# Optimization experiments

Hardware: AMD Instinct MI355X
Metric: run time of the kernel (lower is better)

Reference implementation:

```python
import jax, jax.numpy as jnp
import numpy as np

KH = KW = 3
K = KH * KW
STRIDE = 1
PAD = 1
DIL = 1
GROUPS = 1
DG = 1  # deformable_groups
CIN = 256
COUT = 256
DC = 64  # depth_channels


def conv2d(x, w, b):
    out = jax.lax.conv_general_dilated(
        x, w, (STRIDE, STRIDE), [(PAD, PAD), (PAD, PAD)],
        rhs_dilation=(DIL, DIL), dimension_numbers=('NCHW', 'OIHW', 'NCHW'))
    return out + b[None, :, None, None]


def deform_sample(x, offset, mask):
    """Modulated deformable im2col. x:[N,C,H,W], offset:[N,DG*2*K,Ho,Wo],
    mask:[N,DG*K,Ho,Wo] or None. Returns cols [N,C,K,Ho,Wo]."""
    N, C, H, W = x.shape
    Ho = (H + 2 * PAD - (DIL * (KH - 1) + 1)) // STRIDE + 1
    Wo = (W + 2 * PAD - (DIL * (KW - 1) + 1)) // STRIDE + 1
    ky, kx = jnp.meshgrid(jnp.arange(KH), jnp.arange(KW), indexing='ij')
    # base sampling grid per kernel tap: [K,Ho,Wo]
    base_y = (jnp.arange(Ho) * STRIDE - PAD)[None, :, None] + (ky.reshape(-1) * DIL)[:, None, None]
    base_x = (jnp.arange(Wo) * STRIDE - PAD)[None, None, :] + (kx.reshape(-1) * DIL)[:, None, None]
    off = offset.reshape(N, DG, K, 2, Ho, Wo)  # [...,0]=dy, [...,1]=dx (CUDA layout)
    y = base_y[None, None].astype(x.dtype) + off[:, :, :, 0]
    xx = base_x[None, None].astype(x.dtype) + off[:, :, :, 1]
    y0 = jnp.floor(y)
    x0 = jnp.floor(xx)
    ly = y - y0
    lx = xx - x0
    y0i = y0.astype(jnp.int32)
    x0i = x0.astype(jnp.int32)
    xg = x.reshape(N, DG, C // DG, H * W)

    def gather(iy, ix):
        valid = ((iy >= 0) & (iy < H) & (ix >= 0) & (ix < W)).astype(x.dtype)
        idx = (jnp.clip(iy, 0, H - 1) * W + jnp.clip(ix, 0, W - 1)).reshape(N, DG, 1, K * Ho * Wo)
        v = jnp.take_along_axis(xg, idx, axis=3).reshape(N, DG, C // DG, K, Ho, Wo)
        return v * valid[:, :, None]

    v00 = gather(y0i, x0i)
    v01 = gather(y0i, x0i + 1)
    v10 = gather(y0i + 1, x0i)
    v11 = gather(y0i + 1, x0i + 1)
    w00 = (1 - ly) * (1 - lx)
    w01 = (1 - ly) * lx
    w10 = ly * (1 - lx)
    w11 = ly * lx
    cols = (v00 * w00[:, :, None] + v01 * w01[:, :, None]
            + v10 * w10[:, :, None] + v11 * w11[:, :, None])
    if mask is not None:
        cols = cols * mask.reshape(N, DG, 1, K, Ho, Wo)
    return cols.reshape(N, C, K, Ho, Wo)


def deform_conv2d(x, offset, mask, weight, bias):
    cols = deform_sample(x, offset, mask)  # [N,C,K,Ho,Wo]
    N, C, _, Ho, Wo = cols.shape
    Cout = weight.shape[0]
    cg = C // GROUPS
    cols = cols.reshape(N, GROUPS, cg * K, Ho * Wo)
    wg = weight.reshape(GROUPS, Cout // GROUPS, cg * K)
    out = jnp.einsum('gok,ngkp->ngop', wg, cols).reshape(N, Cout, Ho, Wo)
    return out + bias[None, :, None, None]


def setup_inputs() -> dict:
    key = jax.random.key(0)
    ks = jax.random.split(key, 8)
    x = jax.random.normal(ks[0], (4, CIN, 64, 64), dtype=jnp.float32)
    depth = jax.random.normal(ks[1], (4, DC, 64, 64), dtype=jnp.float32)
    stdv = 1.0 / np.sqrt(CIN * KH * KW)
    weight = jax.random.uniform(ks[2], (COUT, CIN // GROUPS, KH, KW), minval=-stdv, maxval=stdv, dtype=jnp.float32)
    bias = jnp.zeros((COUT,), jnp.float32)
    # offset/mask convs are zero-init in the module; use small random weights
    # so the irregular gather path is actually exercised.
    off_w = 0.05 * jax.random.normal(ks[3], (DG * 2 * K, CIN + DC, KH, KW), dtype=jnp.float32)
    off_b = 0.05 * jax.random.normal(ks[4], (DG * 2 * K,), dtype=jnp.float32)
    mask_w = 0.05 * jax.random.normal(ks[5], (DG * K, DC, KH, KW), dtype=jnp.float32)
    mask_b = 0.05 * jax.random.normal(ks[6], (DG * K,), dtype=jnp.float32)
    return {"x": x, "depth": depth, "weight": weight, "bias": bias,
            "off_w": off_w, "off_b": off_b, "mask_w": mask_w, "mask_b": mask_b}


def reference(x, depth, weight, bias, off_w, off_b, mask_w, mask_b):
    # offset = conv_offset(cat(x, depth))
    offset = conv2d(jnp.concatenate([x, depth], axis=1), off_w, off_b)
    # mask = sigmoid(DeformConv(depth, offset))  (non-modulated deform conv)
    mask = jax.nn.sigmoid(deform_conv2d(depth, offset, None, mask_w, mask_b))
    # modulated deformable conv on x
    return deform_conv2d(x, offset, mask, weight, bias)
```

## Files before the change

kernel.cpp:

```cpp
#include <hip/hip_runtime.h>


typedef __bf16 bf16x8 __attribute__((ext_vector_type(8)));
typedef float f32x4 __attribute__((ext_vector_type(4)));
typedef float float2_u __attribute__((ext_vector_type(2), aligned(4)));

__device__ __forceinline__ unsigned short f2bf(float f) {
  unsigned b = __float_as_uint(f);
  return (unsigned short)((b + 0x7fffu + ((b >> 16) & 1u)) >> 16);
}

__global__ __launch_bounds__(256) void k_prep_weight(
    const float* __restrict__ w, unsigned short* __restrict__ wbf)
{
  const int i = blockIdx.x * 256 + threadIdx.x;
  wbf[i] = f2bf(w[i]);
}

__global__ __launch_bounds__(256) void k_offset_conv(
    const float* __restrict__ x, const float* __restrict__ depth,
    const float* __restrict__ off_w, const float* __restrict__ off_b,
    float* __restrict__ offs)
{
  const int seg = blockIdx.x >> 8;
  const int nh  = blockIdx.x & 255;
  const int n = nh >> 6, ho = nh & 63;
  const int tid = threadIdx.x;
  const int lane = tid & 63;
  const int wave = tid >> 6;

  float acc[18];
#pragma unroll
  for (int i = 0; i < 18; ++i) acc[i] = 0.f;

  const int c0 = __builtin_amdgcn_readfirstlane(seg * 80 + wave * 20);

  for (int ci = 0; ci < 20; ++ci) {
    const int c = c0 + ci;
    const float* p = (c < 256) ? (x + (((n << 8) + c) << 12))
                               : (depth + (((n << 6) + (c - 256)) << 12));
    const float v0 = (ho > 0)  ? p[((ho - 1) << 6) + lane] : 0.f;
    const float v1 =             p[( ho      << 6) + lane];
    const float v2 = (ho < 63) ? p[((ho + 1) << 6) + lane] : 0.f;

    float v[9];
#pragma unroll
    for (int ky = 0; ky < 3; ++ky) {
      const float r = (ky == 0) ? v0 : ((ky == 1) ? v1 : v2);
#pragma unroll
      for (int kx = 0; kx < 3; ++kx) {
        const int src = lane + kx - 1;
        const float s = __shfl(r, src & 63);
        v[ky * 3 + kx] = (src >= 0 && src < 64) ? s : 0.f;
      }
    }
    const float* wp = off_w + c * 9;
#pragma unroll
    for (int co = 0; co < 18; ++co) {
      const float* w = wp + co * 2880;
#pragma unroll
      for (int t = 0; t < 9; ++t) acc[co] += v[t] * w[t];
    }
  }

  __shared__ float red[4][18][64];
#pragma unroll
  for (int co = 0; co < 18; ++co) red[wave][co][lane] = acc[co];
  __syncthreads();
  for (int o = tid; o < 18 * 64; o += 256) {
    const int co = o >> 6, wo = o & 63;
    float s = red[0][co][wo] + red[1][co][wo] + red[2][co][wo] + red[3][co][wo];
    if (seg == 0) s += off_b[co];
    atomicAdd(&offs[((n * 18 + co) << 12) + (ho << 6) + wo], s);
  }
}

__global__ __launch_bounds__(512) void k_mask_conv(
    const float* __restrict__ depth, const float* __restrict__ offs,
    const float* __restrict__ mask_w, const float* __restrict__ mask_b,
    float* __restrict__ mask)
{
  const int n  = blockIdx.x >> 6;
  const int ho = blockIdx.x & 63;
  const int tid  = threadIdx.x;
  const int lane = tid & 63;
  const int wave = tid >> 6;
  const int wo = lane;

  int ia[9], ib[9];
  float w0[9], w1[9], w2c[9], w3[9];
  const float* op = offs + ((n * 18) << 12) + (ho << 6) + wo;
#pragma unroll
  for (int k = 0; k < 9; ++k) {
    const float dy = op[(2 * k) << 12];
    const float dx = op[(2 * k + 1) << 12];
    const float yy = (float)(ho - 1 + k / 3) + dy;
    const float xx = (float)(wo - 1 + k % 3) + dx;
    const float y0f = floorf(yy), x0f = floorf(xx);
    const float ly = yy - y0f, lx = xx - x0f;
    const int y0 = (int)y0f, x0 = (int)x0f;
    const int y0c = min(max(y0, 0), 63);
    const int y1c = min(max(y0 + 1, 0), 63);
    const float fy0 = (y0 >= 0 && y0 < 64) ? 1.f : 0.f;
    const float fy1 = (y0 >= -1 && y0 < 63) ? 1.f : 0.f;
    const int x0c = min(max(x0, 0), 63);
    const int x1c = min(max(x0 + 1, 0), 63);
    const int bx  = min(max(x0, 0), 62);
    const float vx0 = (x0 >= 0 && x0 < 64) ? 1.f : 0.f;
    const float vx1 = (x0 >= -1 && x0 < 63) ? 1.f : 0.f;
    const float wl = (1.f - lx) * vx0 * ((x0c == bx) ? 1.f : 0.f)
                   + lx * vx1 * ((x1c == bx) ? 1.f : 0.f);
    const float wr = (1.f - lx) * vx0 * ((x0c == bx + 1) ? 1.f : 0.f)
                   + lx * vx1 * ((x1c == bx + 1) ? 1.f : 0.f);
    const float a0 = (1.f - ly) * fy0;
    const float a1 = ly * fy1;
    ia[k] = ((y0c << 6) + bx) << 2;
    ib[k] = ((y1c << 6) + bx) << 2;
    w0[k] = wl * a0;  w1[k] = wr * a0;
    w2c[k] = wl * a1; w3[k] = wr * a1;
  }

  float acc[9];
#pragma unroll
  for (int i = 0; i < 9; ++i) acc[i] = 0.f;

  const int cbase = __builtin_amdgcn_readfirstlane(wave * 8);
  for (int cc = 0; cc < 8; ++cc) {
    const int c = cbase + cc;
    const char* p = (const char*)(depth + (((n << 6) + c) << 12));
    float val[9];
#pragma unroll
    for (int k = 0; k < 9; ++k) {
      const float2_u A = *(const float2_u*)(p + ia[k]);
      const float2_u B = *(const float2_u*)(p + ib[k]);
      val[k] = A.x * w0[k] + A.y * w1[k] + B.x * w2c[k] + B.y * w3[k];
    }
    const float* wp = mask_w + c * 9;
#pragma unroll
    for (int co = 0; co < 9; ++co) {
#pragma unroll
      for (int k = 0; k < 9; ++k) acc[co] += val[k] * wp[co * 576 + k];
    }
  }

  __shared__ float red[8][9][64];
#pragma unroll
  for (int co = 0; co < 9; ++co) red[wave][co][lane] = acc[co];
  __syncthreads();
  for (int o = tid; o < 9 * 64; o += 512) {
    const int co = o >> 6, w2 = o & 63;
    float s = mask_b[co];
#pragma unroll
    for (int w = 0; w < 8; ++w) s += red[w][co][w2];
    mask[((n * 9 + co) << 12) + (ho << 6) + w2] = 1.f / (1.f + expf(-s));
  }
}

__device__ __forceinline__ void stage_channel_row(const float* src, char* dstb,
                                                  int lane) {
  const char* s = (const char*)src + lane * 4;
#pragma unroll
  for (int j = 0; j < 32; ++j)
    __builtin_amdgcn_global_load_lds(
        (const __attribute__((address_space(1))) void*)(s + j * 256),
        (__attribute__((address_space(3))) void*)(dstb + j * 272), 4, 0, 0);
}

__global__ __launch_bounds__(512, 2) void k_deform_gemm(
    const float* __restrict__ x, const float* __restrict__ offs,
    const float* __restrict__ mask, const unsigned short* __restrict__ wbf,
    const float* __restrict__ bias, float* __restrict__ out)
{
  __shared__ float strip[9 * 2176];
  __shared__ __align__(16) unsigned short Bs[64][72];
  __shared__ float4 pwT[9][64];
  __shared__ int    piT[9][64];

  const int tid = threadIdx.x;
  const int b    = blockIdx.x;
  const int xcd  = b & 7, bslot = b >> 3;
  const int n    = xcd >> 1;
  const int ho   = ((xcd & 1) << 5) + bslot;
  const int pxb  = ho << 6;
  const int ylo  = min(max(ho - 15, 0), 32);

  const int pxl  = tid & 63;
  const int oct  = tid >> 6;
  const int lane = tid & 63;
  const int mrow = lane & 15;
  const int koct = lane >> 4;
  const float* xn = x + ((long)(n << 8) << 12);
  const char* xnc = (const char*)xn;
  char* stripc = (char*)strip;

  stage_channel_row(xn + (oct << 12) + (ylo << 6), stripc + oct * 8704, lane);
  int c_staged = 8;

  for (int e = tid; e < 576; e += 512) {
    const int tap = e >> 6, pl = e & 63;
    const int wo = pl;
    const float dy = offs[((n * 18 + 2 * tap) << 12) + pxb + pl];
    const float dx = offs[((n * 18 + 2 * tap + 1) << 12) + pxb + pl];
    const float m  = mask[((n * 9 + tap) << 12) + pxb + pl];
    const float yy = (float)(ho - 1 + tap / 3) + dy;
    const float xx = (float)(wo - 1 + tap % 3) + dx;
    const float y0f = floorf(yy), x0f = floorf(xx);
    const float ly = yy - y0f, lx = xx - x0f;
    const int y0 = (int)y0f, x0 = (int)x0f;
    const int y0c = min(max(y0, 0), 63);
    const int y1c = min(max(y0 + 1, 0), 63);
    const float fy0 = (y0 >= 0 && y0 < 64) ? 1.f : 0.f;
    const float fy1 = (y0 >= -1 && y0 < 63) ? 1.f : 0.f;
    const int x0c = min(max(x0, 0), 63);
    const int x1c = min(max(x0 + 1, 0), 63);
    const int bx  = min(max(x0, 0), 62);
    const float vx0 = (x0 >= 0 && x0 < 64) ? 1.f : 0.f;
    const float vx1 = (x0 >= -1 && x0 < 63) ? 1.f : 0.f;
    const float wl = (1.f - lx) * vx0 * ((x0c == bx) ? 1.f : 0.f)
                   + lx * vx1 * ((x1c == bx) ? 1.f : 0.f);
    const float wr = (1.f - lx) * vx0 * ((x0c == bx + 1) ? 1.f : 0.f)
                   + lx * vx1 * ((x1c == bx + 1) ? 1.f : 0.f);
    const float a0 = (1.f - ly) * fy0 * m;
    const float a1 = ly * fy1 * m;
    pwT[tap][pl] = make_float4(wl * a0, wr * a0, wl * a1, wr * a1);
    const int ry0 = y0c - ylo, ry1 = y1c - ylo;
    const int ry0c = min(max(ry0, 0), 31), ry1c = min(max(ry1, 0), 31);
    const int bad = ((ry0 != ry0c) || (ry1 != ry1c)) ? 1 : 0;
    const int ad0 = ry0c * 272 + (bx << 2);
    const int ad1 = ry1c * 272 + (bx << 2);
    piT[tap][pl] = ad0 | (ad1 << 14) | (bad << 28);
  }
  __syncthreads();

  auto gather = [&](int ic) {
    const int k0 = (ic << 6) + (oct << 3);
    const int c0 = (int)(((unsigned)k0 * 7282u) >> 16);
    int tap = k0 - 9 * c0;
    const int s9 = (int)(((unsigned)c0 * 7282u) >> 16);
    int soff = (c0 - 9 * s9) * 8704;

    __align__(16) unsigned short v[8];
    unsigned badm = 0;
#pragma unroll
    for (int j = 0; j < 8; ++j) {
      const int pk  = piT[tap][pxl];
      const float4 w = pwT[tap][pxl];
      const float2_u A = *(const float2_u*)(stripc + soff + (pk & 16383));
      const float2_u B = *(const float2_u*)(stripc + soff + ((pk >> 14) & 16383));
      v[j] = f2bf(A.x * w.x + A.y * w.y + B.x * w.z + B.y * w.w);
      badm |= ((unsigned)pk >> 28) << j;
      if (++tap == 9) {
        tap = 0;
        soff += 8704; if (soff == 9 * 8704) soff = 0;
      }
    }

    if (__builtin_expect(badm != 0, 0)) {
#pragma unroll
      for (int j = 0; j < 8; ++j) if (badm & (1u << j)) {
        const int k = k0 + j;
        const int c = (int)(((unsigned)k * 7282u) >> 16);
        const int tp = k - 9 * c;
        const float dy = offs[((n * 18 + 2 * tp) << 12) + pxb + pxl];
        const float dx = offs[((n * 18 + 2 * tp + 1) << 12) + pxb + pxl];
        const float m  = mask[((n * 9 + tp) << 12) + pxb + pxl];
        const float yy = (float)(ho - 1 + tp / 3) + dy;
        const float xx = (float)(pxl - 1 + tp % 3) + dx;
        const float y0f = floorf(yy), x0f = floorf(xx);
        const float ly = yy - y0f, lx = xx - x0f;
        const int y0 = (int)y0f, x0 = (int)x0f;
        const int y0c = min(max(y0, 0), 63);
        const int y1c = min(max(y0 + 1, 0), 63);
        const float fy0 = (y0 >= 0 && y0 < 64) ? 1.f : 0.f;
        const float fy1 = (y0 >= -1 && y0 < 63) ? 1.f : 0.f;
        const int x0c = min(max(x0, 0), 63);
        const int x1c = min(max(x0 + 1, 0), 63);
        const int bx  = min(max(x0, 0), 62);
        const float vx0 = (x0 >= 0 && x0 < 64) ? 1.f : 0.f;
        const float vx1 = (x0 >= -1 && x0 < 63) ? 1.f : 0.f;
        const float wl = (1.f - lx) * vx0 * ((x0c == bx) ? 1.f : 0.f)
                       + lx * vx1 * ((x1c == bx) ? 1.f : 0.f);
        const float wr = (1.f - lx) * vx0 * ((x0c == bx + 1) ? 1.f : 0.f)
                       + lx * vx1 * ((x1c == bx + 1) ? 1.f : 0.f);
        const float a0 = (1.f - ly) * fy0 * m;
        const float a1 = ly * fy1 * m;
        const char* pg = xnc + ((long)c << 14);
        const float2_u Ag = *(const float2_u*)(pg + (((y0c << 6) + bx) << 2));
        const float2_u Bg = *(const float2_u*)(pg + (((y1c << 6) + bx) << 2));
        v[j] = f2bf(Ag.x * (wl * a0) + Ag.y * (wr * a0) +
                    Bg.x * (wl * a1) + Bg.y * (wr * a1));
      }
    }
    *(int4*)&Bs[pxl][oct << 3] = *(const int4*)v;
  };

  bf16x8 afc[2][2];
#pragma unroll
  for (int mt = 0; mt < 2; ++mt)
#pragma unroll
    for (int ks = 0; ks < 2; ++ks) {
      const int row = (oct << 5) + (mt << 4) + mrow;
      const int col = (ks << 5) + (koct << 3);
      afc[mt][ks] = *(const bf16x8*)(wbf + row * 2304 + col);
    }

  gather(0);
  __syncthreads();

  f32x4 acc[2][4];
#pragma unroll
  for (int mt = 0; mt < 2; ++mt)
#pragma unroll
    for (int nt = 0; nt < 4; ++nt)
#pragma unroll
      for (int r = 0; r < 4; ++r) acc[mt][nt][r] = 0.f;

  for (int ic = 0; ic < 36; ++ic) {
    if (ic < 35) {
      const int c_end = (64 * ic + 127) / 9;
      const int cw = c_staged + oct;
      if (cw <= c_end) {
        const int slt = cw - 9 * (int)(((unsigned)cw * 7282u) >> 16);
        stage_channel_row(xn + (cw << 12) + (ylo << 6),
                          stripc + slt * 8704, lane);
      }
      c_staged = c_end + 1;
    }

    bf16x8 afn[2][2];
    if (ic < 35) {
      const int kc = (ic + 1) << 6;
#pragma unroll
      for (int mt = 0; mt < 2; ++mt)
#pragma unroll
        for (int ks = 0; ks < 2; ++ks) {
          const int row = (oct << 5) + (mt << 4) + mrow;
          const int col = kc + (ks << 5) + (koct << 3);
          afn[mt][ks] = *(const bf16x8*)(wbf + row * 2304 + col);
        }
    }

#pragma unroll
    for (int ks = 0; ks < 2; ++ks)
#pragma unroll
      for (int nt = 0; nt < 4; ++nt) {
        const bf16x8 bfr =
            *(const bf16x8*)&Bs[(nt << 4) + mrow][(ks << 5) + (koct << 3)];
        acc[0][nt] = __builtin_amdgcn_mfma_f32_16x16x32_bf16(afc[0][ks], bfr,
                                                             acc[0][nt], 0, 0, 0);
        acc[1][nt] = __builtin_amdgcn_mfma_f32_16x16x32_bf16(afc[1][ks], bfr,
                                                             acc[1][nt], 0, 0, 0);
      }

    __syncthreads();
    if (ic < 35) gather(ic + 1);
    __syncthreads();

#pragma unroll
    for (int mt = 0; mt < 2; ++mt)
#pragma unroll
      for (int ks = 0; ks < 2; ++ks) afc[mt][ks] = afn[mt][ks];
  }

#pragma unroll
  for (int mt = 0; mt < 2; ++mt)
#pragma unroll
    for (int nt = 0; nt < 4; ++nt)
#pragma unroll
      for (int r = 0; r < 4; ++r) {
        const int co = (oct << 5) + (mt << 4) + ((lane >> 4) << 2) + r;
        const int pxg = pxb + (nt << 4) + (lane & 15);
        out[(((n << 8) + co) << 12) + pxg] = acc[mt][nt][r] + bias[co];
      }
}

extern "C" void kernel_launch(void* const* d_in, const int* in_sizes, int n_in,
                              void* d_out, int out_size, void* d_ws, size_t ws_size,
                              hipStream_t stream) {
  const float* x      = (const float*)d_in[0];
  const float* depth  = (const float*)d_in[1];
  const float* weight = (const float*)d_in[2];
  const float* bias   = (const float*)d_in[3];
  const float* off_w  = (const float*)d_in[4];
  const float* off_b  = (const float*)d_in[5];
  const float* mask_w = (const float*)d_in[6];
  const float* mask_b = (const float*)d_in[7];
  float* out = (float*)d_out;

  float* offs = (float*)d_ws;
  float* mask = offs + 294912;
  unsigned short* wbf = (unsigned short*)(mask + 147456);

  hipMemsetAsync(offs, 0, 294912 * sizeof(float), stream);
  k_prep_weight<<<2304, 256, 0, stream>>>(weight, wbf);
  k_offset_conv<<<1024, 256, 0, stream>>>(x, depth, off_w, off_b, offs);
  k_mask_conv<<<256, 512, 0, stream>>>(depth, offs, mask_w, mask_b, mask);
  k_deform_gemm<<<256, 512, 0, stream>>>(x, offs, mask, wbf, bias, out);
}
```

Baseline: 243.7 us.

## Fuse weight prep into offset conv and mask conv into deform GEMM

Merges the bf16 weight conversion into the offset-conv kernel and drops the split-channel atomics and memset by giving each block all 320 channels across 8 waves. The mask deformable conv plus sigmoid is computed inside the GEMM kernel per output row and kept in LDS, so the global mask buffer and two launches go away. The cost is fewer, longer offset-conv blocks (256 instead of 1024) and extra serial work at the start of each GEMM block, with LDS pooled and aliased to fit.

```diff
diff --git a/kernel.cpp b/kernel.cpp
--- a/kernel.cpp
+++ b/kernel.cpp
@@ -10,22 +10,17 @@
   return (unsigned short)((b + 0x7fffu + ((b >> 16) & 1u)) >> 16);
 }
 
-__global__ __launch_bounds__(256) void k_prep_weight(
-    const float* __restrict__ w, unsigned short* __restrict__ wbf)
+__global__ __launch_bounds__(512) void k_prep_offset(
+    const float* __restrict__ x, const float* __restrict__ depth,
+    const float* __restrict__ w, const float* __restrict__ off_w,
+    const float* __restrict__ off_b,
+    unsigned short* __restrict__ wbf, float* __restrict__ offs)
 {
-  const int i = blockIdx.x * 256 + threadIdx.x;
-  wbf[i] = f2bf(w[i]);
-}
-
-__global__ __launch_bounds__(256) void k_offset_conv(
-    const float* __restrict__ x, const float* __restrict__ depth,
-    const float* __restrict__ off_w, const float* __restrict__ off_b,
-    float* __restrict__ offs)
-{
-  const int seg = blockIdx.x >> 8;
-  const int nh  = blockIdx.x & 255;
-  const int n = nh >> 6, ho = nh & 63;
   const int tid = threadIdx.x;
+  for (int i = blockIdx.x * 512 + tid; i < 589824; i += 131072)
+    wbf[i] = f2bf(w[i]);
+
+  const int n = blockIdx.x >> 6, ho = blockIdx.x & 63;
   const int lane = tid & 63;
   const int wave = tid >> 6;
 
@@ -33,9 +28,9 @@
 #pragma unroll
   for (int i = 0; i < 18; ++i) acc[i] = 0.f;
 
-  const int c0 = __builtin_amdgcn_readfirstlane(seg * 80 + wave * 20);
-
-  for (int ci = 0; ci < 20; ++ci) {
+  const int c0 = __builtin_amdgcn_readfirstlane(wave * 40);
+
+  for (int ci = 0; ci < 40; ++ci) {
     const int c = c0 + ci;
     const float* p = (c < 256) ? (x + (((n << 8) + c) << 12))
                                : (depth + (((n << 6) + (c - 256)) << 12));
@@ -57,102 +52,22 @@
     const float* wp = off_w + c * 9;
 #pragma unroll
     for (int co = 0; co < 18; ++co) {
-      const float* w = wp + co * 2880;
-#pragma unroll
-      for (int t = 0; t < 9; ++t) acc[co] += v[t] * w[t];
-    }
-  }
-
-  __shared__ float red[4][18][64];
+      const float* ww = wp + co * 2880;
+#pragma unroll
+      for (int t = 0; t < 9; ++t) acc[co] += v[t] * ww[t];
+    }
+  }
+
+  __shared__ float red[8][18][64];
 #pragma unroll
   for (int co = 0; co < 18; ++co) red[wave][co][lane] = acc[co];
   __syncthreads();
-  for (int o = tid; o < 18 * 64; o += 256) {
+  for (int o = tid; o < 18 * 64; o += 512) {
     const int co = o >> 6, wo = o & 63;
-    float s = red[0][co][wo] + red[1][co][wo] + red[2][co][wo] + red[3][co][wo];
-    if (seg == 0) s += off_b[co];
-    atomicAdd(&offs[((n * 18 + co) << 12) + (ho << 6) + wo], s);
-  }
-}
-
-__global__ __launch_bounds__(512) void k_mask_conv(
-    const float* __restrict__ depth, const float* __restrict__ offs,
-    const float* __restrict__ mask_w, const float* __restrict__ mask_b,
-    float* __restrict__ mask)
-{
-  const int n  = blockIdx.x >> 6;
-  const int ho = blockIdx.x & 63;
-  const int tid  = threadIdx.x;
-  const int lane = tid & 63;
-  const int wave = tid >> 6;
-  const int wo = lane;
-
-  int ia[9], ib[9];
-  float w0[9], w1[9], w2c[9], w3[9];
-  const float* op = offs + ((n * 18) << 12) + (ho << 6) + wo;
-#pragma unroll
-  for (int k = 0; k < 9; ++k) {
-    const float dy = op[(2 * k) << 12];
-    const float dx = op[(2 * k + 1) << 12];
-    const float yy = (float)(ho - 1 + k / 3) + dy;
-    const float xx = (float)(wo - 1 + k % 3) + dx;
-    const float y0f = floorf(yy), x0f = floorf(xx);
-    const float ly = yy - y0f, lx = xx - x0f;
-    const int y0 = (int)y0f, x0 = (int)x0f;
-    const int y0c = min(max(y0, 0), 63);
-    const int y1c = min(max(y0 + 1, 0), 63);
-    const float fy0 = (y0 >= 0 && y0 < 64) ? 1.f : 0.f;
-    const float fy1 = (y0 >= -1 && y0 < 63) ? 1.f : 0.f;
-    const int x0c = min(max(x0, 0), 63);
-    const int x1c = min(max(x0 + 1, 0), 63);
-    const int bx  = min(max(x0, 0), 62);
-    const float vx0 = (x0 >= 0 && x0 < 64) ? 1.f : 0.f;
-    const float vx1 = (x0 >= -1 && x0 < 63) ? 1.f : 0.f;
-    const float wl = (1.f - lx) * vx0 * ((x0c == bx) ? 1.f : 0.f)
-                   + lx * vx1 * ((x1c == bx) ? 1.f : 0.f);
-    const float wr = (1.f - lx) * vx0 * ((x0c == bx + 1) ? 1.f : 0.f)
-                   + lx * vx1 * ((x1c == bx + 1) ? 1.f : 0.f);
-    const float a0 = (1.f - ly) * fy0;
-    const float a1 = ly * fy1;
-    ia[k] = ((y0c << 6) + bx) << 2;
-    ib[k] = ((y1c << 6) + bx) << 2;
-    w0[k] = wl * a0;  w1[k] = wr * a0;
-    w2c[k] = wl * a1; w3[k] = wr * a1;
-  }
-
-  float acc[9];
-#pragma unroll
-  for (int i = 0; i < 9; ++i) acc[i] = 0.f;
-
-  const int cbase = __builtin_amdgcn_readfirstlane(wave * 8);
-  for (int cc = 0; cc < 8; ++cc) {
-    const int c = cbase + cc;
-    const char* p = (const char*)(depth + (((n << 6) + c) << 12));
-    float val[9];
-#pragma unroll
-    for (int k = 0; k < 9; ++k) {
-      const float2_u A = *(const float2_u*)(p + ia[k]);
-      const float2_u B = *(const float2_u*)(p + ib[k]);
-      val[k] = A.x * w0[k] + A.y * w1[k] + B.x * w2c[k] + B.y * w3[k];
-    }
-    const float* wp = mask_w + c * 9;
-#pragma unroll
-    for (int co = 0; co < 9; ++co) {
-#pragma unroll
-      for (int k = 0; k < 9; ++k) acc[co] += val[k] * wp[co * 576 + k];
-    }
-  }
-
-  __shared__ float red[8][9][64];
-#pragma unroll
-  for (int co = 0; co < 9; ++co) red[wave][co][lane] = acc[co];
-  __syncthreads();
-  for (int o = tid; o < 9 * 64; o += 512) {
-    const int co = o >> 6, w2 = o & 63;
-    float s = mask_b[co];
-#pragma unroll
-    for (int w = 0; w < 8; ++w) s += red[w][co][w2];
-    mask[((n * 9 + co) << 12) + (ho << 6) + w2] = 1.f / (1.f + expf(-s));
+    float s = off_b[co];
+#pragma unroll
+    for (int wv = 0; wv < 8; ++wv) s += red[wv][co][wo];
+    offs[((n * 18 + co) << 12) + (ho << 6) + wo] = s;
   }
 }
 
@@ -166,15 +81,19 @@
         (__attribute__((address_space(3))) void*)(dstb + j * 272), 4, 0, 0);
 }
 
-__global__ __launch_bounds__(512, 2) void k_deform_gemm(
-    const float* __restrict__ x, const float* __restrict__ offs,
-    const float* __restrict__ mask, const unsigned short* __restrict__ wbf,
+__global__ __launch_bounds__(512, 2) void k_fused_gemm(
+    const float* __restrict__ x, const float* __restrict__ depth,
+    const float* __restrict__ offs, const float* __restrict__ mask_w,
+    const float* __restrict__ mask_b, const unsigned short* __restrict__ wbf,
     const float* __restrict__ bias, float* __restrict__ out)
 {
-  __shared__ float strip[9 * 2176];
-  __shared__ __align__(16) unsigned short Bs[64][72];
-  __shared__ float4 pwT[9][64];
-  __shared__ int    piT[9][64];
+  __shared__ __align__(16) char pool[101376];
+  char* stripc = pool;
+  unsigned short (*Bs)[72]  = (unsigned short (*)[72])(pool + 78336);
+  float4 (*pwT)[64]         = (float4 (*)[64])(pool + 87552);
+  int (*piT)[64]            = (int (*)[64])(pool + 96768);
+  float (*mskL)[64]         = (float (*)[64])(pool + 99072);
+  float (*red)[9][64]       = (float (*)[9][64])(pool + 78336);
 
   const int tid = threadIdx.x;
   const int b    = blockIdx.x;
@@ -190,18 +109,87 @@
   const int mrow = lane & 15;
   const int koct = lane >> 4;
   const float* xn = x + ((long)(n << 8) << 12);
-  const char* xnc = (const char*)xn;
-  char* stripc = (char*)strip;
 
   stage_channel_row(xn + (oct << 12) + (ylo << 6), stripc + oct * 8704, lane);
   int c_staged = 8;
+
+  {
+    const int wo = lane;
+    int ia[9], ib[9];
+    float w0[9], w1[9], w2c[9], w3[9];
+    const float* op = offs + ((n * 18) << 12) + (ho << 6) + wo;
+#pragma unroll
+    for (int k = 0; k < 9; ++k) {
+      const float dy = op[(2 * k) << 12];
+      const float dx = op[(2 * k + 1) << 12];
+      const float yy = (float)(ho - 1 + k / 3) + dy;
+      const float xx = (float)(wo - 1 + k % 3) + dx;
+      const float y0f = floorf(yy), x0f = floorf(xx);
+      const float ly = yy - y0f, lx = xx - x0f;
+      const int y0 = (int)y0f, x0 = (int)x0f;
+      const int y0c = min(max(y0, 0), 63);
+      const int y1c = min(max(y0 + 1, 0), 63);
+      const float fy0 = (y0 >= 0 && y0 < 64) ? 1.f : 0.f;
+      const float fy1 = (y0 >= -1 && y0 < 63) ? 1.f : 0.f;
+      const int x0c = min(max(x0, 0), 63);
+      const int x1c = min(max(x0 + 1, 0), 63);
+      const int bx  = min(max(x0, 0), 62);
+      const float vx0 = (x0 >= 0 && x0 < 64) ? 1.f : 0.f;
+      const float vx1 = (x0 >= -1 && x0 < 63) ? 1.f : 0.f;
+      const float wl = (1.f - lx) * vx0 * ((x0c == bx) ? 1.f : 0.f)
+                     + lx * vx1 * ((x1c == bx) ? 1.f : 0.f);
+      const float wr = (1.f - lx) * vx0 * ((x0c == bx + 1) ? 1.f : 0.f)
+                     + lx * vx1 * ((x1c == bx + 1) ? 1.f : 0.f);
+      const float a0 = (1.f - ly) * fy0;
+      const float a1 = ly * fy1;
+      ia[k] = ((y0c << 6) + bx) << 2;
+      ib[k] = ((y1c << 6) + bx) << 2;
+      w0[k] = wl * a0;  w1[k] = wr * a0;
+      w2c[k] = wl * a1; w3[k] = wr * a1;
+    }
+
+    float acc2[9];
+#pragma unroll
+    for (int i = 0; i < 9; ++i) acc2[i] = 0.f;
+
+    const int cbase = __builtin_amdgcn_readfirstlane(oct * 8);
+    for (int cc = 0; cc < 8; ++cc) {
+      const int c = cbase + cc;
+      const char* p = (const char*)(depth + (((n << 6) + c) << 12));
+      float val[9];
+#pragma unroll
+      for (int k = 0; k < 9; ++k) {
+        const float2_u A = *(const float2_u*)(p + ia[k]);
+        const float2_u B = *(const float2_u*)(p + ib[k]);
+        val[k] = A.x * w0[k] + A.y * w1[k] + B.x * w2c[k] + B.y * w3[k];
+      }
+      const float* wp = mask_w + c * 9;
+#pragma unroll
+      for (int co = 0; co < 9; ++co) {
+#pragma unroll
+        for (int k = 0; k < 9; ++k) acc2[co] += val[k] * wp[co * 576 + k];
+      }
+    }
+#pragma unroll
+    for (int co = 0; co < 9; ++co) red[oct][co][lane] = acc2[co];
+  }
+  __syncthreads();
+
+  for (int o = tid; o < 576; o += 512) {
+    const int co = o >> 6, wo = o & 63;
+    float s = mask_b[co];
+#pragma unroll
+    for (int wv = 0; wv < 8; ++wv) s += red[wv][co][wo];
+    mskL[co][wo] = 1.f / (1.f + expf(-s));
+  }
+  __syncthreads();
 
   for (int e = tid; e < 576; e += 512) {
     const int tap = e >> 6, pl = e & 63;
     const int wo = pl;
     const float dy = offs[((n * 18 + 2 * tap) << 12) + pxb + pl];
     const float dx = offs[((n * 18 + 2 * tap + 1) << 12) + pxb + pl];
-    const float m  = mask[((n * 9 + tap) << 12) + pxb + pl];
+    const float m  = mskL[tap][pl];
     const float yy = (float)(ho - 1 + tap / 3) + dy;
     const float xx = (float)(wo - 1 + tap % 3) + dx;
     const float y0f = floorf(yy), x0f = floorf(xx);
@@ -263,7 +251,7 @@
         const int tp = k - 9 * c;
         const float dy = offs[((n * 18 + 2 * tp) << 12) + pxb + pxl];
         const float dx = offs[((n * 18 + 2 * tp + 1) << 12) + pxb + pxl];
-        const float m  = mask[((n * 9 + tp) << 12) + pxb + pxl];
+        const float m  = mskL[tp][pxl];
         const float yy = (float)(ho - 1 + tp / 3) + dy;
         const float xx = (float)(pxl - 1 + tp % 3) + dx;
         const float y0f = floorf(yy), x0f = floorf(xx);
@@ -284,7 +272,7 @@
                        + lx * vx1 * ((x1c == bx + 1) ? 1.f : 0.f);
         const float a0 = (1.f - ly) * fy0 * m;
         const float a1 = ly * fy1 * m;
-        const char* pg = xnc + ((long)c << 14);
+        const char* pg = (const char*)xn + ((long)c << 14);
         const float2_u Ag = *(const float2_u*)(pg + (((y0c << 6) + bx) << 2));
         const float2_u Bg = *(const float2_u*)(pg + (((y1c << 6) + bx) << 2));
         v[j] = f2bf(Ag.x * (wl * a0) + Ag.y * (wr * a0) +
@@ -388,12 +376,10 @@
   float* out = (float*)d_out;
 
   float* offs = (float*)d_ws;
-  float* mask = offs + 294912;
-  unsigned short* wbf = (unsigned short*)(mask + 147456);
-
-  hipMemsetAsync(offs, 0, 294912 * sizeof(float), stream);
-  k_prep_weight<<<2304, 256, 0, stream>>>(weight, wbf);
-  k_offset_conv<<<1024, 256, 0, stream>>>(x, depth, off_w, off_b, offs);
-  k_mask_conv<<<256, 512, 0, stream>>>(depth, offs, mask_w, mask_b, mask);
-  k_deform_gemm<<<256, 512, 0, stream>>>(x, offs, mask, wbf, bias, out);
-}
+  unsigned short* wbf = (unsigned short*)(offs + 294912);
+
+  k_prep_offset<<<256, 512, 0, stream>>>(x, depth, weight, off_w, off_b,
+                                         wbf, offs);
+  k_fused_gemm<<<256, 512, 0, stream>>>(x, depth, offs, mask_w, mask_b,
+                                        wbf, bias, out);
+}
```

After: 259.9 us. 6.6% more time.
